# Optimization experiments

Measured on AMD Instinct MI355X. Metric: run time of the kernel, lower is better.

Reference implementation:

```python
import jax, jax.numpy as jnp
import numpy as np

MAX_DEGREE = 7  # selected_degree for every neuron (== config.max_degree)


def _cheb_combine(alpha, coeffs):
    """sum_d coeffs[:, d] * T_d(alpha) via the Chebyshev recurrence.

    alpha:  [B, out]
    coeffs: [out, D+1]
    returns [B, out]
    """
    t_m2 = jnp.ones_like(alpha)          # T_0
    t_m1 = alpha                          # T_1
    acc = coeffs[:, 0] + coeffs[:, 1] * alpha

    def body(carry, c_d):                 # c_d: [out]
        tm2, tm1, a = carry
        t = 2.0 * alpha * tm1 - tm2       # T_d recurrence
        return (tm1, t, a + c_d * t), None

    (_, _, acc), _ = jax.lax.scan(body, (t_m2, t_m1, acc), coeffs[:, 2:].T)
    return acc


def _kan_layer(x, w, b, coeffs, cW, cb):
    # w: [out, in] (stacked per-neuron projection vectors), b: [out]
    alpha = x @ w.T + b                   # [B, out] -- per-neuron scalar projection
    neuron_out = _cheb_combine(alpha, coeffs)  # [B, out]
    return neuron_out @ cW + cb           # combine_W [out,out], combin_b [out]


def setup_inputs() -> dict:
    key = jax.random.key(0)
    ks = jax.random.split(key, 12)
    B = 16384
    shape = [1024, 1024, 256]
    D1 = MAX_DEGREE + 1
    inp = {"x": jax.random.normal(ks[0], (B, shape[0]), dtype=jnp.float32)}
    ki = 1
    for li, (din, dout) in enumerate(zip(shape[:-1], shape[1:]), start=1):
        inp[f"w{li}"] = jax.random.normal(ks[ki], (dout, din), dtype=jnp.float32) / np.sqrt(din); ki += 1
        inp[f"b{li}"] = jnp.zeros((dout,), dtype=jnp.float32)
        inp[f"coeffs{li}"] = jax.random.normal(ks[ki], (dout, D1), dtype=jnp.float32) * 0.1; ki += 1
        inp[f"cW{li}"] = jnp.eye(dout, dtype=jnp.float32)
        inp[f"cb{li}"] = jnp.zeros((dout,), dtype=jnp.float32)
    return inp


def reference(x, w1, b1, coeffs1, cW1, cb1, w2, b2, coeffs2, cW2, cb2):
    h = _kan_layer(x, w1, b1, coeffs1, cW1, cb1)
    return _kan_layer(h, w2, b2, coeffs2, cW2, cb2)
```

## Files before the change

kernel.cpp:

```cpp
#include <hip/hip_runtime.h>


typedef __attribute__((ext_vector_type(8))) short short8;
typedef __attribute__((ext_vector_type(4))) float f32x4;
typedef unsigned short ushort_t;

#define GAS(p) ((const __attribute__((address_space(1))) void*)(p))
#define LAS(p) ((__attribute__((address_space(3))) void*)(p))

__device__ __forceinline__ void split2(float f, ushort_t& h, ushort_t& l) {
    const unsigned u = __float_as_uint(f);
    h = (ushort_t)(u >> 16);
    const float hf = __uint_as_float(u & 0xFFFF0000u);
    l = (ushort_t)(__float_as_uint(f - hf) >> 16);
}

__global__ __launch_bounds__(256) void split_f32(const float* __restrict__ src,
                                                 ushort_t* __restrict__ hi,
                                                 ushort_t* __restrict__ lo, int n4) {
    const int i = blockIdx.x * 256 + threadIdx.x;
    if (i >= n4) return;
    const float4 v = ((const float4*)src)[i];
    ushort4 h, l;
    split2(v.x, h.x, l.x); split2(v.y, h.y, l.y);
    split2(v.z, h.z, l.z); split2(v.w, h.w, l.w);
    ((ushort4*)hi)[i] = h;
    ((ushort4*)lo)[i] = l;
}

__global__ __launch_bounds__(256) void bias2eff_kernel(const float* __restrict__ cb1,
                                                       const float* __restrict__ w2,
                                                       const float* __restrict__ b2,
                                                       float* __restrict__ out) {
    const int wave = threadIdx.x >> 6, lane = threadIdx.x & 63;
    const int n = blockIdx.x * 4 + wave;
    const float4* row = (const float4*)(w2 + (size_t)n * 1024);
    const float4* c4  = (const float4*)cb1;
    float s = 0.f;
#pragma unroll
    for (int i = 0; i < 4; ++i) {
        const int idx = lane + i * 64;
        const float4 a = row[idx], c = c4[idx];
        s += a.x * c.x + a.y * c.y + a.z * c.z + a.w * c.w;
    }
#pragma unroll
    for (int off = 32; off; off >>= 1) s += __shfl_down(s, off);
    if (lane == 0) out[n] = s + b2[n];
}

__global__ __launch_bounds__(256) void tsplit_kernel(const float* __restrict__ src,
                                                     ushort_t* __restrict__ hiT,
                                                     ushort_t* __restrict__ loT) {
    const int i = blockIdx.x * 256 + threadIdx.x;
    const int r = i >> 8, c = i & 255;
    ushort_t h, l;
    split2(src[r * 256 + c], h, l);
    hiT[c * 256 + r] = h;
    loT[c * 256 + r] = l;
}

constexpr int PKT = 16;
__global__ __launch_bounds__(256)
void prep_gemm_sk(const float* __restrict__ A, const float* __restrict__ W,
                  float* __restrict__ Cp, int M, int N, int K, int KS) {
    __shared__ float As[PKT][68];
    __shared__ float Bs[PKT][68];
    const int tid = threadIdx.x;
    const int bn = blockIdx.x, bm = blockIdx.y, bz = blockIdx.z;
    const int kc = K / KS, k0 = bz * kc;
    const int tx = tid & 15, ty = tid >> 4;
    float acc[4][4];
#pragma unroll
    for (int i = 0; i < 4; ++i)
#pragma unroll
        for (int j = 0; j < 4; ++j) acc[i][j] = 0.f;
    const float* Ab = A + (size_t)(bm * 64) * K + k0;
    const float* Wb = W + (size_t)(bn * 64) * K + k0;
    const int sr = tid >> 2;
    const int sc = (tid & 3) * 4;
    for (int kt = 0; kt < kc; kt += PKT) {
        const float4 va = *(const float4*)(Ab + (size_t)sr * K + kt + sc);
        As[sc + 0][sr] = va.x; As[sc + 1][sr] = va.y; As[sc + 2][sr] = va.z; As[sc + 3][sr] = va.w;
        const float4 vb = *(const float4*)(Wb + (size_t)sr * K + kt + sc);
        Bs[sc + 0][sr] = vb.x; Bs[sc + 1][sr] = vb.y; Bs[sc + 2][sr] = vb.z; Bs[sc + 3][sr] = vb.w;
        __syncthreads();
#pragma unroll
        for (int k = 0; k < PKT; ++k) {
            const float4 a4 = *(const float4*)&As[k][ty * 4];
            const float4 b4 = *(const float4*)&Bs[k][tx * 4];
            const float a[4] = {a4.x, a4.y, a4.z, a4.w};
            const float b[4] = {b4.x, b4.y, b4.z, b4.w};
#pragma unroll
            for (int i = 0; i < 4; ++i)
#pragma unroll
                for (int j = 0; j < 4; ++j) acc[i][j] = fmaf(a[i], b[j], acc[i][j]);
        }
        __syncthreads();
    }
    float* Cb = Cp + (size_t)bz * M * N + (size_t)(bm * 64 + ty * 4) * N + bn * 64 + tx * 4;
#pragma unroll
    for (int i = 0; i < 4; ++i)
        *(float4*)(Cb + (size_t)i * N) = make_float4(acc[i][0], acc[i][1], acc[i][2], acc[i][3]);
}

__global__ __launch_bounds__(256)
void combine_split(const float* __restrict__ Cp, ushort_t* __restrict__ hi,
                   ushort_t* __restrict__ lo, int n4, int KS) {
    const int i = blockIdx.x * 256 + threadIdx.x;
    if (i >= n4) return;
    float4 s = ((const float4*)Cp)[i];
    for (int z = 1; z < KS; ++z) {
        const float4 v = ((const float4*)Cp)[(size_t)z * n4 + i];
        s.x += v.x; s.y += v.y; s.z += v.z; s.w += v.w;
    }
    ushort4 h, l;
    split2(s.x, h.x, l.x); split2(s.y, h.y, l.y);
    split2(s.z, h.z, l.z); split2(s.w, h.w, l.w);
    ((ushort4*)hi)[i] = h;
    ((ushort4*)lo)[i] = l;
}

__global__ __launch_bounds__(512, 2)
void kan_mfma256(const ushort_t* __restrict__ Ahg,
                 const ushort_t* __restrict__ Alg,
                 const ushort_t* __restrict__ Bhg,
                 const ushort_t* __restrict__ Blg,
                 const float* __restrict__ bias,
                 const float* __restrict__ coeffs,
                 ushort_t* __restrict__ Chh,
                 ushort_t* __restrict__ Chl,
                 int M, int N, int K)
{
    __shared__ __align__(16) ushort_t LDS[2][4][256 * 32];

    const int tid  = threadIdx.x;
    const int lane = tid & 63;
    const int wave = tid >> 6;

    const int gx  = gridDim.x;
    const int nwg = gx * gridDim.y;
    int wg = blockIdx.y * gx + blockIdx.x;
    wg = (wg & 7) * (nwg >> 3) + (wg >> 3);
    const int bn = wg % gx;
    const int bm = wg / gx;

    const int wm = wave >> 2;
    const int wn = wave & 3;
    const int lr = lane & 15;
    const int lg = lane >> 4;

    const int sg  = wave & 3;
    const int r0a = (wave >> 2) * 128;
    const size_t aRow0 = (size_t)bm * 256;
    const size_t bRow0 = (size_t)bn * 256;

    f32x4 acc[8][4];
#pragma unroll
    for (int m = 0; m < 8; ++m)
#pragma unroll
        for (int n = 0; n < 4; ++n) acc[m][n] = f32x4{0.f, 0.f, 0.f, 0.f};

    auto stage = [&](int q, int s, int kt) {
        const int r0 = r0a + ((q & 1) ? 64 : 0);
        const int lo = (q >= 2) ? 1 : 0;
        const size_t ga = (aRow0 + r0 + lane) * K + kt + sg * 8;
        const size_t gb = (bRow0 + r0 + lane) * K + kt + sg * 8;
        const int di = sg * 2048 + r0 * 8;
        __builtin_amdgcn_global_load_lds(GAS((lo ? Alg : Ahg) + ga),
                                         LAS(&LDS[s][lo][di]), 16, 0, 0);
        __builtin_amdgcn_global_load_lds(GAS((lo ? Blg : Bhg) + gb),
                                         LAS(&LDS[s][2 + lo][di]), 16, 0, 0);
    };

#pragma unroll
    for (int q = 0; q < 4; ++q) stage(q, 0, 0);
    asm volatile("s_waitcnt vmcnt(0)" ::: "memory");
    __builtin_amdgcn_s_barrier();

    const int nt = K >> 5;
    constexpr int MH[4] = {0, 1, 1, 0};
    constexpr int NH[4] = {0, 0, 1, 1};

    for (int t = 0; t < nt; ++t) {
        const int cur = t & 1;
        const int kt_next = (t + 1) << 5;
        const bool more = (t + 1) < nt;

#pragma unroll
        for (int q = 0; q < 4; ++q) {
            const int mh = MH[q], nh = NH[q];
            short8 ah[4], al4[4], bh2[2], bl2[2];
#pragma unroll
            for (int m = 0; m < 4; ++m) {
                const int idx = lg * 2048 + (wm * 128 + (mh * 4 + m) * 16 + lr) * 8;
                ah[m]  = *(const short8*)&LDS[cur][0][idx];
                al4[m] = *(const short8*)&LDS[cur][1][idx];
            }
#pragma unroll
            for (int n = 0; n < 2; ++n) {
                const int idx = lg * 2048 + (wn * 64 + (nh * 2 + n) * 16 + lr) * 8;
                bh2[n] = *(const short8*)&LDS[cur][2][idx];
                bl2[n] = *(const short8*)&LDS[cur][3][idx];
            }
            if (more) stage(q, cur ^ 1, kt_next);

            __builtin_amdgcn_s_barrier();
            asm volatile("s_waitcnt lgkmcnt(0)" ::: "memory");
            __builtin_amdgcn_sched_barrier(0);
            __builtin_amdgcn_s_setprio(1);
#pragma unroll
            for (int m = 0; m < 4; ++m)
#pragma unroll
                for (int n = 0; n < 2; ++n) {
                    const int am = mh * 4 + m, an = nh * 2 + n;
                    acc[am][an] = __builtin_amdgcn_mfma_f32_16x16x32_bf16(ah[m],  bh2[n], acc[am][an], 0, 0, 0);
                    acc[am][an] = __builtin_amdgcn_mfma_f32_16x16x32_bf16(ah[m],  bl2[n], acc[am][an], 0, 0, 0);
                    acc[am][an] = __builtin_amdgcn_mfma_f32_16x16x32_bf16(al4[m], bh2[n], acc[am][an], 0, 0, 0);
                }
            __builtin_amdgcn_s_setprio(0);
            __builtin_amdgcn_s_barrier();
        }

        if (more) {
            asm volatile("s_waitcnt vmcnt(0)" ::: "memory");
            __builtin_amdgcn_s_barrier();
        }
    }

    const int gm0 = bm * 256 + wm * 128;
    const int gn0 = bn * 256 + wn * 64;
#pragma unroll
    for (int n = 0; n < 4; ++n) {
        const int colg = gn0 + n * 16 + lr;
        const float bia = bias[colg];
        float cf[8];
        {
            const float4 u0 = *(const float4*)(coeffs + (size_t)colg * 8);
            const float4 u1 = *(const float4*)(coeffs + (size_t)colg * 8 + 4);
            cf[0] = u0.x; cf[1] = u0.y; cf[2] = u0.z; cf[3] = u0.w;
            cf[4] = u1.x; cf[5] = u1.y; cf[6] = u1.z; cf[7] = u1.w;
        }
#pragma unroll
        for (int m = 0; m < 8; ++m) {
            const int rowb = gm0 + m * 16 + lg * 4;
#pragma unroll
            for (int j = 0; j < 4; ++j) {
                const float alpha = acc[m][n][j] + bia;
                float tm2 = 1.f, tm1 = alpha;
                float v = fmaf(cf[1], alpha, cf[0]);
#pragma unroll
                for (int d = 2; d < 8; ++d) {
                    const float tch = 2.f * alpha * tm1 - tm2;
                    v = fmaf(cf[d], tch, v);
                    tm2 = tm1; tm1 = tch;
                }
                const size_t o = (size_t)(rowb + j) * N + colg;
                ushort_t h, l2;
                split2(v, h, l2);
                Chh[o] = h; Chl[o] = l2;
            }
        }
    }
}

template<bool CHEB, bool OUT_F32>
__global__ __launch_bounds__(256)
void kan_mfma(const ushort_t* __restrict__ Ahg,
              const ushort_t* __restrict__ Alg,
              const ushort_t* __restrict__ Bhg,
              const ushort_t* __restrict__ Blg,
              const float* __restrict__ bias,
              const float* __restrict__ coeffs,
              float* __restrict__ Cf,
              ushort_t* __restrict__ Chh,
              ushort_t* __restrict__ Chl,
              int M, int N, int K)
{
    __shared__ __align__(16) ushort_t Ah[128 * 32];
    __shared__ __align__(16) ushort_t Al[128 * 32];
    __shared__ __align__(16) ushort_t Bh[128 * 32];
    __shared__ __align__(16) ushort_t Bl[128 * 32];

    const int tid  = threadIdx.x;
    const int lane = tid & 63;
    const int wave = tid >> 6;

    const int gx = gridDim.x;
    const int nwg = gx * gridDim.y;
    int wg = blockIdx.y * gx + blockIdx.x;
    wg = (wg & 7) * (nwg >> 3) + (wg >> 3);
    const int bn = wg % gx;
    const int bm = wg / gx;

    const int wm = wave >> 1, wn = wave & 1;
    const int lr = lane & 15;
    const int lg = lane >> 4;

    f32x4 acc[4][4];
#pragma unroll
    for (int m = 0; m < 4; ++m)
#pragma unroll
        for (int n = 0; n < 4; ++n) acc[m][n] = f32x4{0.f, 0.f, 0.f, 0.f};

    const size_t aRow0 = (size_t)(bm * 128);
    const size_t bRow0 = (size_t)(bn * 128);
    const int g = wave;
    const int ldsb = g * 1024;

    for (int kt = 0; kt < K; kt += 32) {
#pragma unroll
        for (int r0 = 0; r0 < 128; r0 += 64) {
            const size_t goA = (aRow0 + r0 + lane) * K + kt + g * 8;
            const size_t goB = (bRow0 + r0 + lane) * K + kt + g * 8;
            __builtin_amdgcn_global_load_lds(GAS(Ahg + goA), LAS(&Ah[ldsb + r0 * 8]), 16, 0, 0);
            __builtin_amdgcn_global_load_lds(GAS(Alg + goA), LAS(&Al[ldsb + r0 * 8]), 16, 0, 0);
            __builtin_amdgcn_global_load_lds(GAS(Bhg + goB), LAS(&Bh[ldsb + r0 * 8]), 16, 0, 0);
            __builtin_amdgcn_global_load_lds(GAS(Blg + goB), LAS(&Bl[ldsb + r0 * 8]), 16, 0, 0);
        }
        __syncthreads();

        short8 a_h[4], a_l[4], b_h[4], b_l[4];
#pragma unroll
        for (int m = 0; m < 4; ++m) {
            const int off = lg * 1024 + (wm * 64 + m * 16 + lr) * 8;
            a_h[m] = *(const short8*)&Ah[off];
            a_l[m] = *(const short8*)&Al[off];
        }
#pragma unroll
        for (int n = 0; n < 4; ++n) {
            const int off = lg * 1024 + (wn * 64 + n * 16 + lr) * 8;
            b_h[n] = *(const short8*)&Bh[off];
            b_l[n] = *(const short8*)&Bl[off];
        }
#pragma unroll
        for (int m = 0; m < 4; ++m)
#pragma unroll
            for (int n = 0; n < 4; ++n) {
                acc[m][n] = __builtin_amdgcn_mfma_f32_16x16x32_bf16(a_h[m], b_h[n], acc[m][n], 0, 0, 0);
                acc[m][n] = __builtin_amdgcn_mfma_f32_16x16x32_bf16(a_h[m], b_l[n], acc[m][n], 0, 0, 0);
                acc[m][n] = __builtin_amdgcn_mfma_f32_16x16x32_bf16(a_l[m], b_h[n], acc[m][n], 0, 0, 0);
            }
        __syncthreads();
    }

    const int gm0 = bm * 128 + wm * 64;
    const int gn0 = bn * 128 + wn * 64;
#pragma unroll
    for (int n = 0; n < 4; ++n) {
        const int colg = gn0 + n * 16 + lr;
        const float bia = bias[colg];
        float cf[8];
        if constexpr (CHEB) {
            const float4 u0 = *(const float4*)(coeffs + (size_t)colg * 8);
            const float4 u1 = *(const float4*)(coeffs + (size_t)colg * 8 + 4);
            cf[0] = u0.x; cf[1] = u0.y; cf[2] = u0.z; cf[3] = u0.w;
            cf[4] = u1.x; cf[5] = u1.y; cf[6] = u1.z; cf[7] = u1.w;
        }
#pragma unroll
        for (int m = 0; m < 4; ++m) {
            const int rowb = gm0 + m * 16 + lg * 4;
#pragma unroll
            for (int j = 0; j < 4; ++j) {
                const float alpha = acc[m][n][j] + bia;
                float v;
                if constexpr (CHEB) {
                    float tm2 = 1.f, tm1 = alpha;
                    v = fmaf(cf[1], alpha, cf[0]);
#pragma unroll
                    for (int d = 2; d < 8; ++d) {
                        const float t = 2.f * alpha * tm1 - tm2;
                        v = fmaf(cf[d], t, v);
                        tm2 = tm1; tm1 = t;
                    }
                } else {
                    v = alpha;
                }
                const size_t o = (size_t)(rowb + j) * N + colg;
                if constexpr (OUT_F32) {
                    Cf[o] = v;
                } else {
                    ushort_t h, l2;
                    split2(v, h, l2);
                    Chh[o] = h; Chl[o] = l2;
                }
            }
        }
    }
}

extern "C" void kernel_launch(void* const* d_in, const int* in_sizes, int n_in,
                              void* d_out, int out_size, void* d_ws, size_t ws_size,
                              hipStream_t stream) {
    const float* x       = (const float*)d_in[0];
    const float* w1      = (const float*)d_in[1];
    const float* b1      = (const float*)d_in[2];
    const float* coeffs1 = (const float*)d_in[3];
    const float* cW1     = (const float*)d_in[4];
    const float* cb1     = (const float*)d_in[5];
    const float* w2      = (const float*)d_in[6];
    const float* b2      = (const float*)d_in[7];
    const float* coeffs2 = (const float*)d_in[8];
    const float* cW2     = (const float*)d_in[9];
    const float* cb2     = (const float*)d_in[10];

    constexpr int B  = 16384;
    constexpr int D1 = 1024;
    constexpr int D2 = 256;
    constexpr int KS = 4;

    char* w = (char*)d_ws;
    size_t off = 0;
    auto alloc = [&](size_t bytes) { char* p = w + off; off += (bytes + 255) & ~(size_t)255; return p; };
    ushort_t* xh   = (ushort_t*)alloc((size_t)B * D1 * 2);
    ushort_t* xl   = (ushort_t*)alloc((size_t)B * D1 * 2);
    ushort_t* hh   = (ushort_t*)alloc((size_t)B * D1 * 2);
    ushort_t* hl   = (ushort_t*)alloc((size_t)B * D1 * 2);
    ushort_t* ph   = (ushort_t*)alloc((size_t)B * D2 * 2);
    ushort_t* pl   = (ushort_t*)alloc((size_t)B * D2 * 2);
    ushort_t* w1h  = (ushort_t*)alloc((size_t)D1 * D1 * 2);
    ushort_t* w1l  = (ushort_t*)alloc((size_t)D1 * D1 * 2);
    float*    m2p  = (float*)alloc((size_t)KS * D2 * D1 * 4);
    ushort_t* m2h  = (ushort_t*)alloc((size_t)D2 * D1 * 2);
    ushort_t* m2l  = (ushort_t*)alloc((size_t)D2 * D1 * 2);
    ushort_t* cw2h = (ushort_t*)alloc((size_t)D2 * D2 * 2);
    ushort_t* cw2l = (ushort_t*)alloc((size_t)D2 * D2 * 2);
    float*    b2e  = (float*)alloc(D2 * 4);

    split_f32<<<dim3(B * D1 / 4 / 256), dim3(256), 0, stream>>>(x, xh, xl, B * D1 / 4);
    split_f32<<<dim3(D1 * D1 / 4 / 256), dim3(256), 0, stream>>>(w1, w1h, w1l, D1 * D1 / 4);
    prep_gemm_sk<<<dim3(D1 / 64, D2 / 64, KS), dim3(256), 0, stream>>>(w2, cW1, m2p, D2, D1, D1, KS);
    combine_split<<<dim3(D2 * D1 / 4 / 256), dim3(256), 0, stream>>>(m2p, m2h, m2l, D2 * D1 / 4, KS);
    bias2eff_kernel<<<dim3(D2 / 4), dim3(256), 0, stream>>>(cb1, w2, b2, b2e);
    tsplit_kernel<<<dim3(D2 * D2 / 256), dim3(256), 0, stream>>>(cW2, cw2h, cw2l);

    kan_mfma256<<<dim3(D1 / 256, B / 256), dim3(512), 0, stream>>>(
        xh, xl, w1h, w1l, b1, coeffs1, hh, hl, B, D1, D1);
    kan_mfma<true, false><<<dim3(D2 / 128, B / 128), dim3(256), 0, stream>>>(
        hh, hl, m2h, m2l, b2e, coeffs2, nullptr, ph, pl, B, D2, D1);
    kan_mfma<false, true><<<dim3(D2 / 128, B / 128), dim3(256), 0, stream>>>(
        ph, pl, cw2h, cw2l, cb2, nullptr, (float*)d_out, nullptr, nullptr, B, D2, D2);
}
```

Measured before the change: 355.0 us.

## Double-buffer kan_mfma, restructure 256-tile main loop, and fuse small prep kernels

The 128-tile kan_mfma kernel gets a two-stage LDS double buffer, so the next K-tile's global-to-LDS loads are issued before the current tile's MFMAs, and it drops one of its two barriers per iteration. The 256-tile kernel now issues all prefetch loads at the start of each iteration, loads B fragments once, and runs two M-half MFMA clusters without the intermediate barriers. Several small prep kernels (the x/w1 split, combine, transpose-split and bias fold) are merged into fewer launches to cut launch overhead. The double buffer doubles LDS use in kan_mfma, and the loop changes raise register pressure, which may limit occupancy.

```diff
diff --git a/kernel.cpp b/kernel.cpp
--- a/kernel.cpp
+++ b/kernel.cpp
@@ -15,48 +15,19 @@
     l = (ushort_t)(__float_as_uint(f - hf) >> 16);
 }
 
-__global__ __launch_bounds__(256) void split_f32(const float* __restrict__ src,
-                                                 ushort_t* __restrict__ hi,
-                                                 ushort_t* __restrict__ lo, int n4) {
-    const int i = blockIdx.x * 256 + threadIdx.x;
-    if (i >= n4) return;
+__global__ __launch_bounds__(256)
+void fused_split(const float* __restrict__ x, ushort_t* __restrict__ xh, ushort_t* __restrict__ xl,
+                 const float* __restrict__ w1, ushort_t* __restrict__ w1h, ushort_t* __restrict__ w1l) {
+    const int bid = blockIdx.x;
+    const float* src; ushort_t* hi; ushort_t* lo; int i;
+    if (bid < 16384) { src = x;  hi = xh;  lo = xl;  i = bid * 256 + threadIdx.x; }
+    else             { src = w1; hi = w1h; lo = w1l; i = (bid - 16384) * 256 + threadIdx.x; }
     const float4 v = ((const float4*)src)[i];
     ushort4 h, l;
     split2(v.x, h.x, l.x); split2(v.y, h.y, l.y);
     split2(v.z, h.z, l.z); split2(v.w, h.w, l.w);
     ((ushort4*)hi)[i] = h;
     ((ushort4*)lo)[i] = l;
-}
-
-__global__ __launch_bounds__(256) void bias2eff_kernel(const float* __restrict__ cb1,
-                                                       const float* __restrict__ w2,
-                                                       const float* __restrict__ b2,
-                                                       float* __restrict__ out) {
-    const int wave = threadIdx.x >> 6, lane = threadIdx.x & 63;
-    const int n = blockIdx.x * 4 + wave;
-    const float4* row = (const float4*)(w2 + (size_t)n * 1024);
-    const float4* c4  = (const float4*)cb1;
-    float s = 0.f;
-#pragma unroll
-    for (int i = 0; i < 4; ++i) {
-        const int idx = lane + i * 64;
-        const float4 a = row[idx], c = c4[idx];
-        s += a.x * c.x + a.y * c.y + a.z * c.z + a.w * c.w;
-    }
-#pragma unroll
-    for (int off = 32; off; off >>= 1) s += __shfl_down(s, off);
-    if (lane == 0) out[n] = s + b2[n];
-}
-
-__global__ __launch_bounds__(256) void tsplit_kernel(const float* __restrict__ src,
-                                                     ushort_t* __restrict__ hiT,
-                                                     ushort_t* __restrict__ loT) {
-    const int i = blockIdx.x * 256 + threadIdx.x;
-    const int r = i >> 8, c = i & 255;
-    ushort_t h, l;
-    split2(src[r * 256 + c], h, l);
-    hiT[c * 256 + r] = h;
-    loT[c * 256 + r] = l;
 }
 
 constexpr int PKT = 16;
@@ -104,20 +75,47 @@
 }
 
 __global__ __launch_bounds__(256)
-void combine_split(const float* __restrict__ Cp, ushort_t* __restrict__ hi,
-                   ushort_t* __restrict__ lo, int n4, int KS) {
-    const int i = blockIdx.x * 256 + threadIdx.x;
-    if (i >= n4) return;
-    float4 s = ((const float4*)Cp)[i];
-    for (int z = 1; z < KS; ++z) {
-        const float4 v = ((const float4*)Cp)[(size_t)z * n4 + i];
-        s.x += v.x; s.y += v.y; s.z += v.z; s.w += v.w;
-    }
-    ushort4 h, l;
-    split2(s.x, h.x, l.x); split2(s.y, h.y, l.y);
-    split2(s.z, h.z, l.z); split2(s.w, h.w, l.w);
-    ((ushort4*)hi)[i] = h;
-    ((ushort4*)lo)[i] = l;
+void prep_small(const float* __restrict__ m2p, ushort_t* __restrict__ m2h, ushort_t* __restrict__ m2l,
+                const float* __restrict__ cW2, ushort_t* __restrict__ cw2h, ushort_t* __restrict__ cw2l,
+                const float* __restrict__ cb1, const float* __restrict__ w2,
+                const float* __restrict__ b2, float* __restrict__ b2e) {
+    const int bid = blockIdx.x;
+    if (bid < 256) {
+        const int i = bid * 256 + threadIdx.x;
+        float4 s = ((const float4*)m2p)[i];
+#pragma unroll
+        for (int z = 1; z < 4; ++z) {
+            const float4 v = ((const float4*)m2p)[(size_t)z * 65536 + i];
+            s.x += v.x; s.y += v.y; s.z += v.z; s.w += v.w;
+        }
+        ushort4 h, l;
+        split2(s.x, h.x, l.x); split2(s.y, h.y, l.y);
+        split2(s.z, h.z, l.z); split2(s.w, h.w, l.w);
+        ((ushort4*)m2h)[i] = h;
+        ((ushort4*)m2l)[i] = l;
+    } else if (bid < 512) {
+        const int i = (bid - 256) * 256 + threadIdx.x;
+        const int r = i >> 8, c = i & 255;
+        ushort_t h, l;
+        split2(cW2[r * 256 + c], h, l);
+        cw2h[c * 256 + r] = h;
+        cw2l[c * 256 + r] = l;
+    } else {
+        const int wave = threadIdx.x >> 6, lane = threadIdx.x & 63;
+        const int n = (bid - 512) * 4 + wave;
+        const float4* row = (const float4*)(w2 + (size_t)n * 1024);
+        const float4* c4  = (const float4*)cb1;
+        float s = 0.f;
+#pragma unroll
+        for (int i = 0; i < 4; ++i) {
+            const int idx = lane + i * 64;
+            const float4 a = row[idx], c = c4[idx];
+            s += a.x * c.x + a.y * c.y + a.z * c.z + a.w * c.w;
+        }
+#pragma unroll
+        for (int off = 32; off; off >>= 1) s += __shfl_down(s, off);
+        if (lane == 0) b2e[n] = s + b2[n];
+    }
 }
 
 __global__ __launch_bounds__(512, 2)
@@ -160,72 +158,71 @@
 #pragma unroll
         for (int n = 0; n < 4; ++n) acc[m][n] = f32x4{0.f, 0.f, 0.f, 0.f};
 
-    auto stage = [&](int q, int s, int kt) {
-        const int r0 = r0a + ((q & 1) ? 64 : 0);
-        const int lo = (q >= 2) ? 1 : 0;
-        const size_t ga = (aRow0 + r0 + lane) * K + kt + sg * 8;
-        const size_t gb = (bRow0 + r0 + lane) * K + kt + sg * 8;
-        const int di = sg * 2048 + r0 * 8;
-        __builtin_amdgcn_global_load_lds(GAS((lo ? Alg : Ahg) + ga),
-                                         LAS(&LDS[s][lo][di]), 16, 0, 0);
-        __builtin_amdgcn_global_load_lds(GAS((lo ? Blg : Bhg) + gb),
-                                         LAS(&LDS[s][2 + lo][di]), 16, 0, 0);
+    auto stage = [&](int s, int kt) {
+#pragma unroll
+        for (int rc = 0; rc < 2; ++rc) {
+            const int r0 = r0a + rc * 64;
+            const size_t ga = (aRow0 + r0 + lane) * K + kt + sg * 8;
+            const size_t gb = (bRow0 + r0 + lane) * K + kt + sg * 8;
+            const int di = sg * 2048 + r0 * 8;
+            __builtin_amdgcn_global_load_lds(GAS(Ahg + ga), LAS(&LDS[s][0][di]), 16, 0, 0);
+            __builtin_amdgcn_global_load_lds(GAS(Alg + ga), LAS(&LDS[s][1][di]), 16, 0, 0);
+            __builtin_amdgcn_global_load_lds(GAS(Bhg + gb), LAS(&LDS[s][2][di]), 16, 0, 0);
+            __builtin_amdgcn_global_load_lds(GAS(Blg + gb), LAS(&LDS[s][3][di]), 16, 0, 0);
+        }
     };
 
-#pragma unroll
-    for (int q = 0; q < 4; ++q) stage(q, 0, 0);
+    stage(0, 0);
     asm volatile("s_waitcnt vmcnt(0)" ::: "memory");
     __builtin_amdgcn_s_barrier();
 
     const int nt = K >> 5;
-    constexpr int MH[4] = {0, 1, 1, 0};
-    constexpr int NH[4] = {0, 0, 1, 1};
+
+#define CLUSTER256(MH)                                                          \
+    {                                                                           \
+        short8 ah[4], al4[4];                                                   \
+        _Pragma("unroll")                                                       \
+        for (int m = 0; m < 4; ++m) {                                           \
+            const int idx = lg * 2048 + (wm * 128 + (MH) * 64 + m * 16 + lr) * 8;\
+            ah[m]  = *(const short8*)&LDS[cur][0][idx];                         \
+            al4[m] = *(const short8*)&LDS[cur][1][idx];                         \
+        }                                                                       \
+        asm volatile("s_waitcnt lgkmcnt(0)" ::: "memory");                      \
+        __builtin_amdgcn_sched_barrier(0);                                      \
+        __builtin_amdgcn_s_setprio(1);                                          \
+        _Pragma("unroll")                                                       \
+        for (int m = 0; m < 4; ++m)                                             \
+            _Pragma("unroll")                                                   \
+            for (int n = 0; n < 4; ++n) {                                       \
+                acc[(MH)*4+m][n] = __builtin_amdgcn_mfma_f32_16x16x32_bf16(ah[m],  bh[n], acc[(MH)*4+m][n], 0, 0, 0); \
+                acc[(MH)*4+m][n] = __builtin_amdgcn_mfma_f32_16x16x32_bf16(ah[m],  bl[n], acc[(MH)*4+m][n], 0, 0, 0); \
+                acc[(MH)*4+m][n] = __builtin_amdgcn_mfma_f32_16x16x32_bf16(al4[m], bh[n], acc[(MH)*4+m][n], 0, 0, 0); \
+            }                                                                   \
+        __builtin_amdgcn_s_setprio(0);                                          \
+    }
 
     for (int t = 0; t < nt; ++t) {
         const int cur = t & 1;
-        const int kt_next = (t + 1) << 5;
         const bool more = (t + 1) < nt;
 
-#pragma unroll
-        for (int q = 0; q < 4; ++q) {
-            const int mh = MH[q], nh = NH[q];
-            short8 ah[4], al4[4], bh2[2], bl2[2];
-#pragma unroll
-            for (int m = 0; m < 4; ++m) {
-                const int idx = lg * 2048 + (wm * 128 + (mh * 4 + m) * 16 + lr) * 8;
-                ah[m]  = *(const short8*)&LDS[cur][0][idx];
-                al4[m] = *(const short8*)&LDS[cur][1][idx];
-            }
-#pragma unroll
-            for (int n = 0; n < 2; ++n) {
-                const int idx = lg * 2048 + (wn * 64 + (nh * 2 + n) * 16 + lr) * 8;
-                bh2[n] = *(const short8*)&LDS[cur][2][idx];
-                bl2[n] = *(const short8*)&LDS[cur][3][idx];
-            }
-            if (more) stage(q, cur ^ 1, kt_next);
-
-            __builtin_amdgcn_s_barrier();
-            asm volatile("s_waitcnt lgkmcnt(0)" ::: "memory");
-            __builtin_amdgcn_sched_barrier(0);
-            __builtin_amdgcn_s_setprio(1);
-#pragma unroll
-            for (int m = 0; m < 4; ++m)
-#pragma unroll
-                for (int n = 0; n < 2; ++n) {
-                    const int am = mh * 4 + m, an = nh * 2 + n;
-                    acc[am][an] = __builtin_amdgcn_mfma_f32_16x16x32_bf16(ah[m],  bh2[n], acc[am][an], 0, 0, 0);
-                    acc[am][an] = __builtin_amdgcn_mfma_f32_16x16x32_bf16(ah[m],  bl2[n], acc[am][an], 0, 0, 0);
-                    acc[am][an] = __builtin_amdgcn_mfma_f32_16x16x32_bf16(al4[m], bh2[n], acc[am][an], 0, 0, 0);
-                }
-            __builtin_amdgcn_s_setprio(0);
-            __builtin_amdgcn_s_barrier();
-        }
+        if (more) stage(cur ^ 1, (t + 1) << 5);
+
+        short8 bh[4], bl[4];
+#pragma unroll
+        for (int n = 0; n < 4; ++n) {
+            const int idx = lg * 2048 + (wn * 64 + n * 16 + lr) * 8;
+            bh[n] = *(const short8*)&LDS[cur][2][idx];
+            bl[n] = *(const short8*)&LDS[cur][3][idx];
+        }
+        CLUSTER256(0)
+        CLUSTER256(1)
 
         if (more) {
             asm volatile("s_waitcnt vmcnt(0)" ::: "memory");
             __builtin_amdgcn_s_barrier();
         }
     }
+#undef CLUSTER256
 
     const int gm0 = bm * 256 + wm * 128;
     const int gn0 = bn * 256 + wn * 64;
@@ -264,7 +261,7 @@
 }
 
 template<bool CHEB, bool OUT_F32>
-__global__ __launch_bounds__(256)
+__global__ __launch_bounds__(256, 2)
 void kan_mfma(const ushort_t* __restrict__ Ahg,
               const ushort_t* __restrict__ Alg,
               const ushort_t* __restrict__ Bhg,
@@ -276,10 +273,7 @@
               ushort_t* __restrict__ Chl,
               int M, int N, int K)
 {
-    __shared__ __align__(16) ushort_t Ah[128 * 32];
-    __shared__ __align__(16) ushort_t Al[128 * 32];
-    __shared__ __align__(16) ushort_t Bh[128 * 32];
-    __shared__ __align__(16) ushort_t Bl[128 * 32];
+    __shared__ __align__(16) ushort_t LDS[2][4][128 * 32];
 
     const int tid  = threadIdx.x;
     const int lane = tid & 63;
@@ -304,34 +298,50 @@
 
     const size_t aRow0 = (size_t)(bm * 128);
     const size_t bRow0 = (size_t)(bn * 128);
-    const int g = wave;
-    const int ldsb = g * 1024;
-
-    for (int kt = 0; kt < K; kt += 32) {
-#pragma unroll
-        for (int r0 = 0; r0 < 128; r0 += 64) {
-            const size_t goA = (aRow0 + r0 + lane) * K + kt + g * 8;
-            const size_t goB = (bRow0 + r0 + lane) * K + kt + g * 8;
-            __builtin_amdgcn_global_load_lds(GAS(Ahg + goA), LAS(&Ah[ldsb + r0 * 8]), 16, 0, 0);
-            __builtin_amdgcn_global_load_lds(GAS(Alg + goA), LAS(&Al[ldsb + r0 * 8]), 16, 0, 0);
-            __builtin_amdgcn_global_load_lds(GAS(Bhg + goB), LAS(&Bh[ldsb + r0 * 8]), 16, 0, 0);
-            __builtin_amdgcn_global_load_lds(GAS(Blg + goB), LAS(&Bl[ldsb + r0 * 8]), 16, 0, 0);
-        }
-        __syncthreads();
+    const int sg = wave;
+    const int ldsb = sg * 1024;
+
+    auto stage = [&](int s, int kt) {
+#pragma unroll
+        for (int rc = 0; rc < 2; ++rc) {
+            const int r0 = rc * 64;
+            const size_t ga = (aRow0 + r0 + lane) * K + kt + sg * 8;
+            const size_t gb = (bRow0 + r0 + lane) * K + kt + sg * 8;
+            const int di = ldsb + r0 * 8;
+            __builtin_amdgcn_global_load_lds(GAS(Ahg + ga), LAS(&LDS[s][0][di]), 16, 0, 0);
+            __builtin_amdgcn_global_load_lds(GAS(Alg + ga), LAS(&LDS[s][1][di]), 16, 0, 0);
+            __builtin_amdgcn_global_load_lds(GAS(Bhg + gb), LAS(&LDS[s][2][di]), 16, 0, 0);
+            __builtin_amdgcn_global_load_lds(GAS(Blg + gb), LAS(&LDS[s][3][di]), 16, 0, 0);
+        }
+    };
+
+    stage(0, 0);
+    asm volatile("s_waitcnt vmcnt(0)" ::: "memory");
+    __builtin_amdgcn_s_barrier();
+
+    const int nt = K >> 5;
+    for (int t = 0; t < nt; ++t) {
+        const int cur = t & 1;
+        const bool more = (t + 1) < nt;
+
+        if (more) stage(cur ^ 1, (t + 1) << 5);
 
         short8 a_h[4], a_l[4], b_h[4], b_l[4];
 #pragma unroll
         for (int m = 0; m < 4; ++m) {
             const int off = lg * 1024 + (wm * 64 + m * 16 + lr) * 8;
-            a_h[m] = *(const short8*)&Ah[off];
-            a_l[m] = *(const short8*)&Al[off];
+            a_h[m] = *(const short8*)&LDS[cur][0][off];
+            a_l[m] = *(const short8*)&LDS[cur][1][off];
         }
 #pragma unroll
         for (int n = 0; n < 4; ++n) {
             const int off = lg * 1024 + (wn * 64 + n * 16 + lr) * 8;
-            b_h[n] = *(const short8*)&Bh[off];
-            b_l[n] = *(const short8*)&Bl[off];
-        }
+            b_h[n] = *(const short8*)&LDS[cur][2][off];
+            b_l[n] = *(const short8*)&LDS[cur][3][off];
+        }
+        asm volatile("s_waitcnt lgkmcnt(0)" ::: "memory");
+        __builtin_amdgcn_sched_barrier(0);
+        __builtin_amdgcn_s_setprio(1);
 #pragma unroll
         for (int m = 0; m < 4; ++m)
 #pragma unroll
@@ -340,7 +350,12 @@
                 acc[m][n] = __builtin_amdgcn_mfma_f32_16x16x32_bf16(a_h[m], b_l[n], acc[m][n], 0, 0, 0);
                 acc[m][n] = __builtin_amdgcn_mfma_f32_16x16x32_bf16(a_l[m], b_h[n], acc[m][n], 0, 0, 0);
             }
-        __syncthreads();
+        __builtin_amdgcn_s_setprio(0);
+
+        if (more) {
+            asm volatile("s_waitcnt vmcnt(0)" ::: "memory");
+            __builtin_amdgcn_s_barrier();
+        }
     }
 
     const int gm0 = bm * 128 + wm * 64;
@@ -368,9 +383,9 @@
                     v = fmaf(cf[1], alpha, cf[0]);
 #pragma unroll
                     for (int d = 2; d < 8; ++d) {
-                        const float t = 2.f * alpha * tm1 - tm2;
-                        v = fmaf(cf[d], t, v);
-                        tm2 = tm1; tm1 = t;
+                        const float t2 = 2.f * alpha * tm1 - tm2;
+                        v = fmaf(cf[d], t2, v);
+                        tm2 = tm1; tm1 = t2;
                     }
                 } else {
                     v = alpha;
@@ -426,12 +441,10 @@
     ushort_t* cw2l = (ushort_t*)alloc((size_t)D2 * D2 * 2);
     float*    b2e  = (float*)alloc(D2 * 4);
 
-    split_f32<<<dim3(B * D1 / 4 / 256), dim3(256), 0, stream>>>(x, xh, xl, B * D1 / 4);
-    split_f32<<<dim3(D1 * D1 / 4 / 256), dim3(256), 0, stream>>>(w1, w1h, w1l, D1 * D1 / 4);
+    fused_split<<<dim3(B * D1 / 4 / 256 + D1 * D1 / 4 / 256), dim3(256), 0, stream>>>(
+        x, xh, xl, w1, w1h, w1l);
     prep_gemm_sk<<<dim3(D1 / 64, D2 / 64, KS), dim3(256), 0, stream>>>(w2, cW1, m2p, D2, D1, D1, KS);
-    combine_split<<<dim3(D2 * D1 / 4 / 256), dim3(256), 0, stream>>>(m2p, m2h, m2l, D2 * D1 / 4, KS);
-    bias2eff_kernel<<<dim3(D2 / 4), dim3(256), 0, stream>>>(cb1, w2, b2, b2e);
-    tsplit_kernel<<<dim3(D2 * D2 / 256), dim3(256), 0, stream>>>(cW2, cw2h, cw2l);
+    prep_small<<<dim3(576), dim3(256), 0, stream>>>(m2p, m2h, m2l, cW2, cw2h, cw2l, cb1, w2, b2, b2e);
 
     kan_mfma256<<<dim3(D1 / 256, B / 256), dim3(512), 0, stream>>>(
         xh, xl, w1h, w1l, b1, coeffs1, hh, hl, B, D1, D1);
```

After: 339.3 us. 1.05x faster.
